# Optimization experiments

Measured on AMD Instinct MI355X. Metric: run time of the kernel, lower is better.

## Reference

```python
import jax, jax.numpy as jnp
import numpy as np

DELTA = 0.1
B, U_DIM, D_DIM, H_DIM, Y_DIM = 4096, 256, 64, 8192, 256
ORDER = H_DIM // 2  # 2x2 rotation blocks


def setup_inputs() -> dict:
    key = jax.random.key(0)
    k = jax.random.split(key, 6)
    u = jax.random.normal(k[0], (B, U_DIM), jnp.float32)
    du = jax.random.normal(k[1], (B, D_DIM), jnp.float32)
    h = jax.random.normal(k[2], (1, H_DIM), jnp.float32)          # h_init state
    # torch.nn.init.uniform_ -> U[0,1); +0.05 keeps 1/omega well-conditioned
    omega = jax.random.uniform(k[3], (ORDER,), jnp.float32) + 0.05
    B_w = jax.random.normal(k[4], (H_DIM, U_DIM + D_DIM), jnp.float32) / np.sqrt(U_DIM + D_DIM)
    C_w = jax.random.normal(k[5], (Y_DIM, H_DIM), jnp.float32) / np.sqrt(H_DIM)
    return {"u": u, "du": du, "h": h, "omega": omega, "B_w": B_w, "C_w": C_w}


def reference(u, du, h, omega, B_w, C_w):
    cos_t = jnp.cos(omega * DELTA)   # [order]
    sin_t = jnp.sin(omega * DELTA)   # [order]
    # exact rotation of state pairs: h viewed as [*, order, 2]
    hp = h.reshape(-1, ORDER, 2)
    h1 = cos_t * hp[..., 0] + sin_t * hp[..., 1]
    h2 = -sin_t * hp[..., 0] + cos_t * hp[..., 1]
    rec = jnp.stack([h1, h2], axis=-1).reshape(h.shape[0], -1)    # [1, h_dim]
    # input projection u_hat = B([du, u])
    udu = jnp.concatenate([du, u], axis=1)                        # [B, d+u]
    u_hat = (udu @ B_w.T).reshape(-1, ORDER, 2)                   # [B, order, 2]
    cm1 = cos_t - 1.0
    inp1 = (sin_t * u_hat[..., 0] - cm1 * u_hat[..., 1]) / omega
    inp2 = (cm1 * u_hat[..., 0] + sin_t * u_hat[..., 1]) / omega
    inp = jnp.stack([inp1, inp2], axis=-1).reshape(udu.shape[0], -1)  # [B, h_dim]
    h_new = rec + inp                                             # broadcast [B, h_dim]
    # sigma = identity, C linear readout (no bias)
    y = h_new @ C_w.T                                             # [B, y_dim]
    return y
```

## Files before the change

### kernel.cpp

```cpp
#include <hip/hip_runtime.h>
#include <hip/hip_bf16.h>

#define BN    4096
#define U_DIM 256
#define D_DIM 64
#define H_DIM 8192
#define Y_DIM 256
#define C_DIM 320
#define DELTAF 0.1f

typedef __bf16 bf16_t;
typedef __attribute__((ext_vector_type(8))) bf16_t bf16x8;
typedef __attribute__((ext_vector_type(4))) float f32x4;

__global__ __launch_bounds__(256) void gemm_E(
    const float* __restrict__ Cw, const float* __restrict__ Bw,
    const float* __restrict__ omega, const float* __restrict__ hin,
    float* __restrict__ E, float* __restrict__ y0) {
  const int b = blockIdx.x;
  const int t = threadIdx.x;
  const int wave = t >> 6, lane = t & 63;
  const int wm = wave >> 1, wn = wave & 1;
  const int l15 = lane & 15, quad = lane >> 4;

  __shared__ bf16_t lA[2][64][40];
  __shared__ bf16_t lB[2][64][40];
  __shared__ __align__(16) float cS[352], cC[352], cI[352];

  const int p = (b * 20) >> 8;
  const int bs = (256 * p + 19) / 20;
  const int P = (256 * (p + 1) + 19) / 20 - bs;
  const int c = b - bs;
  const int it0 = (c * 256) / P;
  const int it1 = ((c + 1) * 256) / P;
  const int k0 = it0 * 32, k1 = it1 * 32;
  const int niter = it1 - it0;
  const int bm = p / 5, bn = p % 5;

  const int npairs = (k1 - k0) >> 1;
  for (int j = t; j < npairs; j += 256) {
    const float om = omega[(k0 >> 1) + j];
    const float ang = om * DELTAF;
    cS[j] = __sinf(ang);
    cC[j] = __cosf(ang) - 1.0f;
    cI[j] = 1.0f / om;
  }
  __syncthreads();

  const int ar = t >> 2, ak = (t & 3) * 8;
  const float* gA = Cw + (size_t)(bm * 64 + ar) * H_DIM + ak;
  const float* gBb = Bw + (size_t)bn * 64 + lane;

  float4 va0, va1, hv0, hv1;
  float bv[8];
  float y0acc = 0.f;

  auto gload = [&](int kk) {
    va0 = *(const float4*)(gA + kk);
    va1 = *(const float4*)(gA + kk + 4);
    const float* pb = gBb + (size_t)(kk + wave * 8) * C_DIM;
#pragma unroll
    for (int j = 0; j < 8; ++j) bv[j] = pb[(size_t)j * C_DIM];
    if (bn == 0) {
      hv0 = *(const float4*)(hin + kk + ak);
      hv1 = *(const float4*)(hin + kk + ak + 4);
    }
  };
  auto stage = [&](int kk, int buf) {
    const int jp = ((kk - k0) >> 1) + (ak >> 1);
    const float4 cs = *(const float4*)&cS[jp];
    const float4 cc = *(const float4*)&cC[jp];
    const float4 ci = *(const float4*)&cI[jp];
    union {
      bf16_t h[8];
      int4 v;
    } pa, pb;
    pa.h[0] = (bf16_t)((va0.x * cs.x + va0.y * cc.x) * ci.x);
    pa.h[1] = (bf16_t)((va0.y * cs.x - va0.x * cc.x) * ci.x);
    pa.h[2] = (bf16_t)((va0.z * cs.y + va0.w * cc.y) * ci.y);
    pa.h[3] = (bf16_t)((va0.w * cs.y - va0.z * cc.y) * ci.y);
    pa.h[4] = (bf16_t)((va1.x * cs.z + va1.y * cc.z) * ci.z);
    pa.h[5] = (bf16_t)((va1.y * cs.z - va1.x * cc.z) * ci.z);
    pa.h[6] = (bf16_t)((va1.z * cs.w + va1.w * cc.w) * ci.w);
    pa.h[7] = (bf16_t)((va1.w * cs.w - va1.z * cc.w) * ci.w);
#pragma unroll
    for (int j = 0; j < 8; ++j) pb.h[j] = (bf16_t)bv[j];
    *(int4*)&lA[buf][ar][ak] = pa.v;
    *(int4*)&lB[buf][lane][wave * 8] = pb.v;
    if (bn == 0) {
      const float c0 = cc.x + 1.f, c1 = cc.y + 1.f;
      const float c2 = cc.z + 1.f, c3 = cc.w + 1.f;
      y0acc += va0.x * (c0 * hv0.x + cs.x * hv0.y) +
               va0.y * (c0 * hv0.y - cs.x * hv0.x) +
               va0.z * (c1 * hv0.z + cs.y * hv0.w) +
               va0.w * (c1 * hv0.w - cs.y * hv0.z) +
               va1.x * (c2 * hv1.x + cs.z * hv1.y) +
               va1.y * (c2 * hv1.y - cs.z * hv1.x) +
               va1.z * (c3 * hv1.z + cs.w * hv1.w) +
               va1.w * (c3 * hv1.w - cs.w * hv1.z);
    }
  };

  f32x4 acc[2][2] = {};
  gload(k0);
  stage(k0, 0);
#pragma unroll 2
  for (int i = 0; i < niter; ++i) {
    __syncthreads();
    const int cur = i & 1;
    if (i + 1 < niter) gload(k0 + (i + 1) * 32);
    const bf16x8 a0 = *(bf16x8*)&lA[cur][wm * 32 + l15][quad * 8];
    const bf16x8 a1 = *(bf16x8*)&lA[cur][wm * 32 + 16 + l15][quad * 8];
    const bf16x8 b0 = *(bf16x8*)&lB[cur][wn * 32 + l15][quad * 8];
    const bf16x8 b1 = *(bf16x8*)&lB[cur][wn * 32 + 16 + l15][quad * 8];
    acc[0][0] = __builtin_amdgcn_mfma_f32_16x16x32_bf16(a0, b0, acc[0][0], 0, 0, 0);
    acc[0][1] = __builtin_amdgcn_mfma_f32_16x16x32_bf16(a0, b1, acc[0][1], 0, 0, 0);
    acc[1][0] = __builtin_amdgcn_mfma_f32_16x16x32_bf16(a1, b0, acc[1][0], 0, 0, 0);
    acc[1][1] = __builtin_amdgcn_mfma_f32_16x16x32_bf16(a1, b1, acc[1][1], 0, 0, 0);
    if (i + 1 < niter) stage(k0 + (i + 1) * 32, cur ^ 1);
  }

#pragma unroll
  for (int mt = 0; mt < 2; ++mt)
#pragma unroll
    for (int nt = 0; nt < 2; ++nt) {
      const int col = bn * 64 + wn * 32 + nt * 16 + l15;
#pragma unroll
      for (int r = 0; r < 4; ++r) {
        const int row = bm * 64 + wm * 32 + mt * 16 + quad * 4 + r;
        atomicAdd(&E[row * C_DIM + col], acc[mt][nt][r]);
      }
    }
  if (bn == 0) {
    y0acc += __shfl_xor(y0acc, 1);
    y0acc += __shfl_xor(y0acc, 2);
    if ((t & 3) == 0) atomicAdd(&y0[bm * 64 + ar], y0acc);
  }
}

__global__ __launch_bounds__(256) void gemm_Y(
    const float* __restrict__ u, const float* __restrict__ du,
    const float* __restrict__ E, const float* __restrict__ y0,
    float* __restrict__ out) {
  const int bm = blockIdx.x;
  const int bn = blockIdx.y;
  const int t = threadIdx.x;
  const int wave = t >> 6, lane = t & 63;
  const int wm = wave >> 1, wn = wave & 1;
  const int l15 = lane & 15, quad = lane >> 4;

  __shared__ bf16_t lA[2][64][40];
  __shared__ bf16_t lB[2][64][40];

  const int ar = t >> 2;
  const int ak = (t & 3) * 8;

  float4 v0, v1, e0, e1;
  auto gload = [&](int kk) {
    const int col = kk + ak;
    if (col < D_DIM) {
      const float* p = du + (size_t)(bm * 64 + ar) * D_DIM + col;
      v0 = *(const float4*)p;
      v1 = *(const float4*)(p + 4);
    } else {
      const float* p = u + (size_t)(bm * 64 + ar) * U_DIM + (col - D_DIM);
      v0 = *(const float4*)p;
      v1 = *(const float4*)(p + 4);
    }
    const float* pe = E + (size_t)(bn * 64 + ar) * C_DIM + col;
    e0 = *(const float4*)pe;
    e1 = *(const float4*)(pe + 4);
  };
  auto stage = [&](int buf) {
    union {
      bf16_t h[8];
      int4 v;
    } pa, pb;
    pa.h[0] = (bf16_t)v0.x; pa.h[1] = (bf16_t)v0.y;
    pa.h[2] = (bf16_t)v0.z; pa.h[3] = (bf16_t)v0.w;
    pa.h[4] = (bf16_t)v1.x; pa.h[5] = (bf16_t)v1.y;
    pa.h[6] = (bf16_t)v1.z; pa.h[7] = (bf16_t)v1.w;
    pb.h[0] = (bf16_t)e0.x; pb.h[1] = (bf16_t)e0.y;
    pb.h[2] = (bf16_t)e0.z; pb.h[3] = (bf16_t)e0.w;
    pb.h[4] = (bf16_t)e1.x; pb.h[5] = (bf16_t)e1.y;
    pb.h[6] = (bf16_t)e1.z; pb.h[7] = (bf16_t)e1.w;
    *(int4*)&lA[buf][ar][ak] = pa.v;
    *(int4*)&lB[buf][ar][ak] = pb.v;
  };

  f32x4 acc[2][2] = {};
  gload(0);
  stage(0);
#pragma unroll
  for (int i = 0; i < 10; ++i) {
    __syncthreads();
    const int cur = i & 1;
    if (i < 9) gload((i + 1) * 32);
    const bf16x8 a0 = *(bf16x8*)&lA[cur][wm * 32 + l15][quad * 8];
    const bf16x8 a1 = *(bf16x8*)&lA[cur][wm * 32 + 16 + l15][quad * 8];
    const bf16x8 b0 = *(bf16x8*)&lB[cur][wn * 32 + l15][quad * 8];
    const bf16x8 b1 = *(bf16x8*)&lB[cur][wn * 32 + 16 + l15][quad * 8];
    acc[0][0] = __builtin_amdgcn_mfma_f32_16x16x32_bf16(a0, b0, acc[0][0], 0, 0, 0);
    acc[0][1] = __builtin_amdgcn_mfma_f32_16x16x32_bf16(a0, b1, acc[0][1], 0, 0, 0);
    acc[1][0] = __builtin_amdgcn_mfma_f32_16x16x32_bf16(a1, b0, acc[1][0], 0, 0, 0);
    acc[1][1] = __builtin_amdgcn_mfma_f32_16x16x32_bf16(a1, b1, acc[1][1], 0, 0, 0);
    if (i < 9) stage(cur ^ 1);
  }
#pragma unroll
  for (int nt = 0; nt < 2; ++nt) {
    const int col = bn * 64 + wn * 32 + nt * 16 + l15;
    const float yc = y0[col];
#pragma unroll
    for (int mt = 0; mt < 2; ++mt) {
#pragma unroll
      for (int r = 0; r < 4; ++r) {
        const int row = bm * 64 + wm * 32 + mt * 16 + quad * 4 + r;
        out[(size_t)row * Y_DIM + col] = acc[mt][nt][r] + yc;
      }
    }
  }
}

extern "C" void kernel_launch(void* const* d_in, const int* in_sizes, int n_in,
                              void* d_out, int out_size, void* d_ws,
                              size_t ws_size, hipStream_t stream) {
  const float* u = (const float*)d_in[0];
  const float* du = (const float*)d_in[1];
  const float* hin = (const float*)d_in[2];
  const float* omega = (const float*)d_in[3];
  const float* Bw = (const float*)d_in[4];
  const float* Cw = (const float*)d_in[5];
  float* out = (float*)d_out;

  char* ws = (char*)d_ws;
  float* E = (float*)ws;
  float* y0 = (float*)(ws + 327680);

  gemm_E<<<256, 256, 0, stream>>>(Cw, Bw, omega, hin, E, y0);
  gemm_Y<<<dim3(BN / 64, Y_DIM / 64), 256, 0, stream>>>(u, du, E, y0, out);
}
```

Baseline: 97.55 us.

## Double K-tile depth to 64 and prefetch two stages ahead in both GEMMs

Both GEMM kernels now process 64-wide K tiles per iteration (two MFMA k-steps per barrier) instead of 32, halving the number of __syncthreads. The global loads are moved to issue right after staging the next tile, so loads for tile i+2 are in flight during compute of tile i+1. This trades more registers and larger LDS tiles for fewer barriers and deeper latency hiding.

```diff
diff --git a/kernel.cpp b/kernel.cpp
--- a/kernel.cpp
+++ b/kernel.cpp
@@ -23,21 +23,21 @@
   const int wm = wave >> 1, wn = wave & 1;
   const int l15 = lane & 15, quad = lane >> 4;
 
-  __shared__ bf16_t lA[2][64][40];
-  __shared__ bf16_t lB[2][64][40];
+  __shared__ bf16_t lA[2][64][72];
+  __shared__ bf16_t lB[2][64][72];
   __shared__ __align__(16) float cS[352], cC[352], cI[352];
 
   const int p = (b * 20) >> 8;
   const int bs = (256 * p + 19) / 20;
   const int P = (256 * (p + 1) + 19) / 20 - bs;
   const int c = b - bs;
-  const int it0 = (c * 256) / P;
-  const int it1 = ((c + 1) * 256) / P;
-  const int k0 = it0 * 32, k1 = it1 * 32;
+  const int it0 = (c * 128) / P;
+  const int it1 = ((c + 1) * 128) / P;
+  const int k0 = it0 * 64;
   const int niter = it1 - it0;
   const int bm = p / 5, bn = p % 5;
 
-  const int npairs = (k1 - k0) >> 1;
+  const int npairs = niter * 32;
   for (int j = t; j < npairs; j += 256) {
     const float om = omega[(k0 >> 1) + j];
     const float ang = om * DELTAF;
@@ -47,77 +47,97 @@
   }
   __syncthreads();
 
-  const int ar = t >> 2, ak = (t & 3) * 8;
+  const int ar = t >> 2, ak = (t & 3) * 16;
   const float* gA = Cw + (size_t)(bm * 64 + ar) * H_DIM + ak;
   const float* gBb = Bw + (size_t)bn * 64 + lane;
 
-  float4 va0, va1, hv0, hv1;
-  float bv[8];
+  float4 va[4], hv[4];
+  float bv[16];
   float y0acc = 0.f;
 
   auto gload = [&](int kk) {
-    va0 = *(const float4*)(gA + kk);
-    va1 = *(const float4*)(gA + kk + 4);
-    const float* pb = gBb + (size_t)(kk + wave * 8) * C_DIM;
-#pragma unroll
-    for (int j = 0; j < 8; ++j) bv[j] = pb[(size_t)j * C_DIM];
+#pragma unroll
+    for (int q = 0; q < 4; ++q)
+      va[q] = *(const float4*)(gA + kk + q * 4);
+    const float* pb = gBb + (size_t)(kk + wave * 16) * C_DIM;
+#pragma unroll
+    for (int j = 0; j < 16; ++j) bv[j] = pb[(size_t)j * C_DIM];
     if (bn == 0) {
-      hv0 = *(const float4*)(hin + kk + ak);
-      hv1 = *(const float4*)(hin + kk + ak + 4);
+#pragma unroll
+      for (int q = 0; q < 4; ++q)
+        hv[q] = *(const float4*)(hin + kk + ak + q * 4);
     }
   };
   auto stage = [&](int kk, int buf) {
     const int jp = ((kk - k0) >> 1) + (ak >> 1);
-    const float4 cs = *(const float4*)&cS[jp];
-    const float4 cc = *(const float4*)&cC[jp];
-    const float4 ci = *(const float4*)&cI[jp];
-    union {
-      bf16_t h[8];
-      int4 v;
-    } pa, pb;
-    pa.h[0] = (bf16_t)((va0.x * cs.x + va0.y * cc.x) * ci.x);
-    pa.h[1] = (bf16_t)((va0.y * cs.x - va0.x * cc.x) * ci.x);
-    pa.h[2] = (bf16_t)((va0.z * cs.y + va0.w * cc.y) * ci.y);
-    pa.h[3] = (bf16_t)((va0.w * cs.y - va0.z * cc.y) * ci.y);
-    pa.h[4] = (bf16_t)((va1.x * cs.z + va1.y * cc.z) * ci.z);
-    pa.h[5] = (bf16_t)((va1.y * cs.z - va1.x * cc.z) * ci.z);
-    pa.h[6] = (bf16_t)((va1.z * cs.w + va1.w * cc.w) * ci.w);
-    pa.h[7] = (bf16_t)((va1.w * cs.w - va1.z * cc.w) * ci.w);
-#pragma unroll
-    for (int j = 0; j < 8; ++j) pb.h[j] = (bf16_t)bv[j];
-    *(int4*)&lA[buf][ar][ak] = pa.v;
-    *(int4*)&lB[buf][lane][wave * 8] = pb.v;
-    if (bn == 0) {
-      const float c0 = cc.x + 1.f, c1 = cc.y + 1.f;
-      const float c2 = cc.z + 1.f, c3 = cc.w + 1.f;
-      y0acc += va0.x * (c0 * hv0.x + cs.x * hv0.y) +
-               va0.y * (c0 * hv0.y - cs.x * hv0.x) +
-               va0.z * (c1 * hv0.z + cs.y * hv0.w) +
-               va0.w * (c1 * hv0.w - cs.y * hv0.z) +
-               va1.x * (c2 * hv1.x + cs.z * hv1.y) +
-               va1.y * (c2 * hv1.y - cs.z * hv1.x) +
-               va1.z * (c3 * hv1.z + cs.w * hv1.w) +
-               va1.w * (c3 * hv1.w - cs.w * hv1.z);
+#pragma unroll
+    for (int h = 0; h < 2; ++h) {
+      const float4 cs = *(const float4*)&cS[jp + h * 4];
+      const float4 cc = *(const float4*)&cC[jp + h * 4];
+      const float4 ci = *(const float4*)&cI[jp + h * 4];
+      const float4 v0 = va[2 * h], v1 = va[2 * h + 1];
+      union {
+        bf16_t x[8];
+        int4 v;
+      } pa;
+      pa.x[0] = (bf16_t)((v0.x * cs.x + v0.y * cc.x) * ci.x);
+      pa.x[1] = (bf16_t)((v0.y * cs.x - v0.x * cc.x) * ci.x);
+      pa.x[2] = (bf16_t)((v0.z * cs.y + v0.w * cc.y) * ci.y);
+      pa.x[3] = (bf16_t)((v0.w * cs.y - v0.z * cc.y) * ci.y);
+      pa.x[4] = (bf16_t)((v1.x * cs.z + v1.y * cc.z) * ci.z);
+      pa.x[5] = (bf16_t)((v1.y * cs.z - v1.x * cc.z) * ci.z);
+      pa.x[6] = (bf16_t)((v1.z * cs.w + v1.w * cc.w) * ci.w);
+      pa.x[7] = (bf16_t)((v1.w * cs.w - v1.z * cc.w) * ci.w);
+      *(int4*)&lA[buf][ar][ak + h * 8] = pa.v;
+      if (bn == 0) {
+        const float4 h0 = hv[2 * h], h1 = hv[2 * h + 1];
+        const float c0 = cc.x + 1.f, c1 = cc.y + 1.f;
+        const float c2 = cc.z + 1.f, c3 = cc.w + 1.f;
+        y0acc += v0.x * (c0 * h0.x + cs.x * h0.y) +
+                 v0.y * (c0 * h0.y - cs.x * h0.x) +
+                 v0.z * (c1 * h0.z + cs.y * h0.w) +
+                 v0.w * (c1 * h0.w - cs.y * h0.z) +
+                 v1.x * (c2 * h1.x + cs.z * h1.y) +
+                 v1.y * (c2 * h1.y - cs.z * h1.x) +
+                 v1.z * (c3 * h1.z + cs.w * h1.w) +
+                 v1.w * (c3 * h1.w - cs.w * h1.z);
+      }
+    }
+#pragma unroll
+    for (int h = 0; h < 2; ++h) {
+      union {
+        bf16_t x[8];
+        int4 v;
+      } pb;
+#pragma unroll
+      for (int j = 0; j < 8; ++j) pb.x[j] = (bf16_t)bv[h * 8 + j];
+      *(int4*)&lB[buf][lane][wave * 16 + h * 8] = pb.v;
     }
   };
 
   f32x4 acc[2][2] = {};
   gload(k0);
   stage(k0, 0);
-#pragma unroll 2
+  if (niter > 1) gload(k0 + 64);
+#pragma unroll 1
   for (int i = 0; i < niter; ++i) {
     __syncthreads();
     const int cur = i & 1;
-    if (i + 1 < niter) gload(k0 + (i + 1) * 32);
-    const bf16x8 a0 = *(bf16x8*)&lA[cur][wm * 32 + l15][quad * 8];
-    const bf16x8 a1 = *(bf16x8*)&lA[cur][wm * 32 + 16 + l15][quad * 8];
-    const bf16x8 b0 = *(bf16x8*)&lB[cur][wn * 32 + l15][quad * 8];
-    const bf16x8 b1 = *(bf16x8*)&lB[cur][wn * 32 + 16 + l15][quad * 8];
-    acc[0][0] = __builtin_amdgcn_mfma_f32_16x16x32_bf16(a0, b0, acc[0][0], 0, 0, 0);
-    acc[0][1] = __builtin_amdgcn_mfma_f32_16x16x32_bf16(a0, b1, acc[0][1], 0, 0, 0);
-    acc[1][0] = __builtin_amdgcn_mfma_f32_16x16x32_bf16(a1, b0, acc[1][0], 0, 0, 0);
-    acc[1][1] = __builtin_amdgcn_mfma_f32_16x16x32_bf16(a1, b1, acc[1][1], 0, 0, 0);
-    if (i + 1 < niter) stage(k0 + (i + 1) * 32, cur ^ 1);
+#pragma unroll
+    for (int kq = 0; kq < 2; ++kq) {
+      const bf16x8 a0 = *(bf16x8*)&lA[cur][wm * 32 + l15][kq * 32 + quad * 8];
+      const bf16x8 a1 = *(bf16x8*)&lA[cur][wm * 32 + 16 + l15][kq * 32 + quad * 8];
+      const bf16x8 b0 = *(bf16x8*)&lB[cur][wn * 32 + l15][kq * 32 + quad * 8];
+      const bf16x8 b1 = *(bf16x8*)&lB[cur][wn * 32 + 16 + l15][kq * 32 + quad * 8];
+      acc[0][0] = __builtin_amdgcn_mfma_f32_16x16x32_bf16(a0, b0, acc[0][0], 0, 0, 0);
+      acc[0][1] = __builtin_amdgcn_mfma_f32_16x16x32_bf16(a0, b1, acc[0][1], 0, 0, 0);
+      acc[1][0] = __builtin_amdgcn_mfma_f32_16x16x32_bf16(a1, b0, acc[1][0], 0, 0, 0);
+      acc[1][1] = __builtin_amdgcn_mfma_f32_16x16x32_bf16(a1, b1, acc[1][1], 0, 0, 0);
+    }
+    if (i + 1 < niter) {
+      stage(k0 + (i + 1) * 64, cur ^ 1);
+      if (i + 2 < niter) gload(k0 + (i + 2) * 64);
+    }
   }
 
 #pragma unroll
@@ -149,62 +169,69 @@
   const int wm = wave >> 1, wn = wave & 1;
   const int l15 = lane & 15, quad = lane >> 4;
 
-  __shared__ bf16_t lA[2][64][40];
-  __shared__ bf16_t lB[2][64][40];
+  __shared__ bf16_t lA[2][64][72];
+  __shared__ bf16_t lB[2][64][72];
 
   const int ar = t >> 2;
-  const int ak = (t & 3) * 8;
-
-  float4 v0, v1, e0, e1;
+  const int ak = (t & 3) * 16;
+
+  float4 va[4], ve[4];
   auto gload = [&](int kk) {
     const int col = kk + ak;
-    if (col < D_DIM) {
-      const float* p = du + (size_t)(bm * 64 + ar) * D_DIM + col;
-      v0 = *(const float4*)p;
-      v1 = *(const float4*)(p + 4);
-    } else {
-      const float* p = u + (size_t)(bm * 64 + ar) * U_DIM + (col - D_DIM);
-      v0 = *(const float4*)p;
-      v1 = *(const float4*)(p + 4);
-    }
+    const float* p = (col < D_DIM)
+                         ? du + (size_t)(bm * 64 + ar) * D_DIM + col
+                         : u + (size_t)(bm * 64 + ar) * U_DIM + (col - D_DIM);
+#pragma unroll
+    for (int q = 0; q < 4; ++q) va[q] = *(const float4*)(p + q * 4);
     const float* pe = E + (size_t)(bn * 64 + ar) * C_DIM + col;
-    e0 = *(const float4*)pe;
-    e1 = *(const float4*)(pe + 4);
+#pragma unroll
+    for (int q = 0; q < 4; ++q) ve[q] = *(const float4*)(pe + q * 4);
   };
   auto stage = [&](int buf) {
-    union {
-      bf16_t h[8];
-      int4 v;
-    } pa, pb;
-    pa.h[0] = (bf16_t)v0.x; pa.h[1] = (bf16_t)v0.y;
-    pa.h[2] = (bf16_t)v0.z; pa.h[3] = (bf16_t)v0.w;
-    pa.h[4] = (bf16_t)v1.x; pa.h[5] = (bf16_t)v1.y;
-    pa.h[6] = (bf16_t)v1.z; pa.h[7] = (bf16_t)v1.w;
-    pb.h[0] = (bf16_t)e0.x; pb.h[1] = (bf16_t)e0.y;
-    pb.h[2] = (bf16_t)e0.z; pb.h[3] = (bf16_t)e0.w;
-    pb.h[4] = (bf16_t)e1.x; pb.h[5] = (bf16_t)e1.y;
-    pb.h[6] = (bf16_t)e1.z; pb.h[7] = (bf16_t)e1.w;
-    *(int4*)&lA[buf][ar][ak] = pa.v;
-    *(int4*)&lB[buf][ar][ak] = pb.v;
+#pragma unroll
+    for (int h = 0; h < 2; ++h) {
+      union {
+        bf16_t x[8];
+        int4 v;
+      } pa, pb;
+      const float4 a0 = va[2 * h], a1 = va[2 * h + 1];
+      const float4 e0 = ve[2 * h], e1 = ve[2 * h + 1];
+      pa.x[0] = (bf16_t)a0.x; pa.x[1] = (bf16_t)a0.y;
+      pa.x[2] = (bf16_t)a0.z; pa.x[3] = (bf16_t)a0.w;
+      pa.x[4] = (bf16_t)a1.x; pa.x[5] = (bf16_t)a1.y;
+      pa.x[6] = (bf16_t)a1.z; pa.x[7] = (bf16_t)a1.w;
+      pb.x[0] = (bf16_t)e0.x; pb.x[1] = (bf16_t)e0.y;
+      pb.x[2] = (bf16_t)e0.z; pb.x[3] = (bf16_t)e0.w;
+      pb.x[4] = (bf16_t)e1.x; pb.x[5] = (bf16_t)e1.y;
+      pb.x[6] = (bf16_t)e1.z; pb.x[7] = (bf16_t)e1.w;
+      *(int4*)&lA[buf][ar][ak + h * 8] = pa.v;
+      *(int4*)&lB[buf][ar][ak + h * 8] = pb.v;
+    }
   };
 
   f32x4 acc[2][2] = {};
   gload(0);
   stage(0);
-#pragma unroll
-  for (int i = 0; i < 10; ++i) {
+  gload(64);
+#pragma unroll
+  for (int i = 0; i < 5; ++i) {
     __syncthreads();
     const int cur = i & 1;
-    if (i < 9) gload((i + 1) * 32);
-    const bf16x8 a0 = *(bf16x8*)&lA[cur][wm * 32 + l15][quad * 8];
-    const bf16x8 a1 = *(bf16x8*)&lA[cur][wm * 32 + 16 + l15][quad * 8];
-    const bf16x8 b0 = *(bf16x8*)&lB[cur][wn * 32 + l15][quad * 8];
-    const bf16x8 b1 = *(bf16x8*)&lB[cur][wn * 32 + 16 + l15][quad * 8];
-    acc[0][0] = __builtin_amdgcn_mfma_f32_16x16x32_bf16(a0, b0, acc[0][0], 0, 0, 0);
-    acc[0][1] = __builtin_amdgcn_mfma_f32_16x16x32_bf16(a0, b1, acc[0][1], 0, 0, 0);
-    acc[1][0] = __builtin_amdgcn_mfma_f32_16x16x32_bf16(a1, b0, acc[1][0], 0, 0, 0);
-    acc[1][1] = __builtin_amdgcn_mfma_f32_16x16x32_bf16(a1, b1, acc[1][1], 0, 0, 0);
-    if (i < 9) stage(cur ^ 1);
+#pragma unroll
+    for (int kq = 0; kq < 2; ++kq) {
+      const bf16x8 a0 = *(bf16x8*)&lA[cur][wm * 32 + l15][kq * 32 + quad * 8];
+      const bf16x8 a1 = *(bf16x8*)&lA[cur][wm * 32 + 16 + l15][kq * 32 + quad * 8];
+      const bf16x8 b0 = *(bf16x8*)&lB[cur][wn * 32 + l15][kq * 32 + quad * 8];
+      const bf16x8 b1 = *(bf16x8*)&lB[cur][wn * 32 + 16 + l15][kq * 32 + quad * 8];
+      acc[0][0] = __builtin_amdgcn_mfma_f32_16x16x32_bf16(a0, b0, acc[0][0], 0, 0, 0);
+      acc[0][1] = __builtin_amdgcn_mfma_f32_16x16x32_bf16(a0, b1, acc[0][1], 0, 0, 0);
+      acc[1][0] = __builtin_amdgcn_mfma_f32_16x16x32_bf16(a1, b0, acc[1][0], 0, 0, 0);
+      acc[1][1] = __builtin_amdgcn_mfma_f32_16x16x32_bf16(a1, b1, acc[1][1], 0, 0, 0);
+    }
+    if (i < 4) {
+      stage(cur ^ 1);
+      if (i < 3) gload((i + 2) * 64);
+    }
   }
 #pragma unroll
   for (int nt = 0; nt < 2; ++nt) {
```

New measurement: 93.89 us. 3.8% less time.
